# Kernel optimization log

Hardware: AMD Instinct MI355X
Metric: run time of the kernel (lower is better)

Reference implementation:

```python
import jax, jax.numpy as jnp
import numpy as np

N_TOTAL = 204800  # total valid nodes across the batch
B = 1024          # number of graphs
D = 512           # input_dim (dim_node)
H = 512           # hidden width of NonLinearClassifier
C = 52            # num_classes
EPS = 1e-5        # BatchNorm eps


def setup_inputs() -> dict:
    key = jax.random.key(0)
    kz, k1, k2, k3 = jax.random.split(key, 4)
    # ragged per-graph node counts summing exactly to N_TOTAL
    rng = np.random.default_rng(0)
    counts = rng.integers(50, 350, size=B).astype(np.float64)
    counts = np.floor(counts * N_TOTAL / counts.sum()).astype(np.int64)
    counts[-1] += N_TOTAL - counts.sum()
    assert counts.min() > 0 and counts.sum() == N_TOTAL
    return {
        "z": jax.random.normal(kz, (N_TOTAL, D), dtype=jnp.float32),
        "batch_num_nodes": jnp.asarray(counts, dtype=jnp.int64),
        "w1": jax.random.normal(k1, (D, H), dtype=jnp.float32) * 0.02,
        "b1": jnp.zeros((H,), jnp.float32),
        "g1": jnp.ones((H,), jnp.float32),
        "beta1": jnp.zeros((H,), jnp.float32),
        "w2": jax.random.normal(k2, (H, H), dtype=jnp.float32) * 0.02,
        "b2": jnp.zeros((H,), jnp.float32),
        "g2": jnp.ones((H,), jnp.float32),
        "beta2": jnp.zeros((H,), jnp.float32),
        "w3": jax.random.normal(k3, (H, C), dtype=jnp.float32) * 0.02,
        "b3": jnp.zeros((C,), jnp.float32),
    }


def _batchnorm(x, gamma, beta):
    # training-mode BatchNorm1d: batch statistics (biased variance)
    m = x.mean(axis=0)
    v = x.var(axis=0)
    return gamma * (x - m) * jax.lax.rsqrt(v + EPS) + beta


def reference(z, batch_num_nodes, w1, b1, g1, beta1, w2, b2, g2, beta2, w3, b3):
    # fused segment-mean pooling (replaces torch.split + per-graph .mean loop)
    seg_ids = jnp.repeat(jnp.arange(B), batch_num_nodes, total_repeat_length=N_TOTAL)
    sums = jax.ops.segment_sum(z, seg_ids, num_segments=B)          # [B, D]
    graph_feats = sums / batch_num_nodes.astype(z.dtype)[:, None]   # [B, D]
    # NonLinearClassifier MLP (dropout inactive in eval / deterministic ref)
    h = jax.nn.relu(_batchnorm(graph_feats @ w1 + b1, g1, beta1))
    h = jax.nn.relu(_batchnorm(h @ w2 + b2, g2, beta2))
    return h @ w3 + b3  # [B, C] logits
```

## Files before the change

kernel.cpp:

```cpp
#include <hip/hip_runtime.h>

#define N_TOTAL 204800
#define NB 1024
#define DIM 512
#define NC 52
#define BN_EPS 1e-5f

__device__ inline void f4add(float4& a, const float4 b) {
    a.x += b.x; a.y += b.y; a.z += b.z; a.w += b.w;
}

__device__ inline float bn_relu1(float v, int f,
                                 const float* __restrict__ s1, const float* __restrict__ s2,
                                 const float* __restrict__ g, const float* __restrict__ beta) {
    float m  = s1[f] * (1.0f / NB);
    float vv = s2[f] * (1.0f / NB) - m * m;
    float is = rsqrtf(vv + BN_EPS);
    float h  = g[f] * (v - m) * is + beta[f];
    return h > 0.f ? h : 0.f;
}

__global__ __launch_bounds__(1024) void k_scan(const int* __restrict__ bnn,
                                               int* __restrict__ offs,
                                               int* __restrict__ cnt,
                                               float* __restrict__ inv,
                                               float* __restrict__ stats ) {
    __shared__ int red[1024];
    int tid = threadIdx.x;
    int v32 = bnn[tid];
    red[tid] = v32;
    __syncthreads();
    for (int s = 512; s > 0; s >>= 1) {
        if (tid < s) red[tid] += red[tid + s];
        __syncthreads();
    }
    int total = red[0];
    __syncthreads();
    int c = (total == N_TOTAL) ? v32 : bnn[2 * tid];
    red[tid] = c;
    __syncthreads();
    for (int off = 1; off < 1024; off <<= 1) {
        int t = (tid >= off) ? red[tid - off] : 0;
        __syncthreads();
        red[tid] += t;
        __syncthreads();
    }
    offs[tid] = red[tid] - c;
    cnt[tid]  = c;
    inv[tid]  = 1.0f / (float)c;
    stats[tid]        = 0.0f;
    stats[tid + 1024] = 0.0f;
}

__global__ __launch_bounds__(256) void k_pool(const float* __restrict__ z,
                                              const int* __restrict__ offs,
                                              const int* __restrict__ cnt,
                                              const float* __restrict__ inv,
                                              float* __restrict__ X) {
    __shared__ float4 buf[3][32];
    int g  = blockIdx.x;
    int cc = blockIdx.y;
    int s0 = offs[g];
    int n  = cnt[g];
    float r = inv[g];
    int tid = threadIdx.x;
    int c4 = tid & 31;
    int rp = tid >> 5;
    const float4* p = (const float4*)z + (size_t)s0 * 128 + cc * 32 + c4;
    float4 a0 = {0,0,0,0}, a1 = {0,0,0,0}, a2 = {0,0,0,0}, a3 = {0,0,0,0};
    int i = rp;
    for (; i + 56 < n; i += 64) {
        float4 v0 = p[(size_t)(i +  0) * 128];
        float4 v1 = p[(size_t)(i +  8) * 128];
        float4 v2 = p[(size_t)(i + 16) * 128];
        float4 v3 = p[(size_t)(i + 24) * 128];
        float4 v4 = p[(size_t)(i + 32) * 128];
        float4 v5 = p[(size_t)(i + 40) * 128];
        float4 v6 = p[(size_t)(i + 48) * 128];
        float4 v7 = p[(size_t)(i + 56) * 128];
        f4add(a0, v0); f4add(a1, v1); f4add(a2, v2); f4add(a3, v3);
        f4add(a0, v4); f4add(a1, v5); f4add(a2, v6); f4add(a3, v7);
    }
    for (; i < n; i += 8) { float4 v = p[(size_t)i * 128]; f4add(a0, v); }
    f4add(a0, a1); f4add(a2, a3); f4add(a0, a2);
    a0.x += __shfl_xor(a0.x, 32); a0.y += __shfl_xor(a0.y, 32);
    a0.z += __shfl_xor(a0.z, 32); a0.w += __shfl_xor(a0.w, 32);
    int w    = tid >> 6;
    int lane = tid & 63;
    if (w > 0 && lane < 32) buf[w - 1][c4] = a0;
    __syncthreads();
    if (w == 0 && lane < 32) {
        f4add(a0, buf[0][c4]); f4add(a0, buf[1][c4]); f4add(a0, buf[2][c4]);
        a0.x *= r; a0.y *= r; a0.z *= r; a0.w *= r;
        ((float4*)X)[(size_t)g * 128 + cc * 32 + c4] = a0;
    }
}

template <bool BNA>
__global__ __launch_bounds__(256) void k_gemm32x64(const float* __restrict__ A,
                                                   const float* __restrict__ W,
                                                   const float* __restrict__ bias,
                                                   const float* __restrict__ ps1,
                                                   const float* __restrict__ ps2,
                                                   const float* __restrict__ gam,
                                                   const float* __restrict__ bet,
                                                   float* __restrict__ Y,
                                                   float* __restrict__ os1,
                                                   float* __restrict__ os2) {
    __shared__ float As[32][34];
    __shared__ float Ws[32][68];
    int tid = threadIdx.x;
    int tx = tid & 15, ty = tid >> 4;
    int gr0 = blockIdx.x * 32;
    int gc0 = blockIdx.y * 64;

    int arow = tid >> 3;
    int akq  = tid & 7;
    int wk0 = tid >> 4;
    int wcq = tid & 15;

    float acc[2][4] = {};

    float4 ra  = *(const float4*)&A[(size_t)(gr0 + arow) * DIM + akq * 4];
    float4 rw0 = *(const float4*)&W[(size_t)wk0 * DIM + gc0 + wcq * 4];
    float4 rw1 = *(const float4*)&W[(size_t)(wk0 + 16) * DIM + gc0 + wcq * 4];

    for (int kt = 0; kt < 16; kt++) {
        float4 v = ra;
        if (BNA) {
            int f0 = kt * 32 + akq * 4;
            v.x = bn_relu1(v.x, f0 + 0, ps1, ps2, gam, bet);
            v.y = bn_relu1(v.y, f0 + 1, ps1, ps2, gam, bet);
            v.z = bn_relu1(v.z, f0 + 2, ps1, ps2, gam, bet);
            v.w = bn_relu1(v.w, f0 + 3, ps1, ps2, gam, bet);
        }
        As[akq * 4 + 0][arow] = v.x;
        As[akq * 4 + 1][arow] = v.y;
        As[akq * 4 + 2][arow] = v.z;
        As[akq * 4 + 3][arow] = v.w;
        *(float4*)&Ws[wk0][wcq * 4]      = rw0;
        *(float4*)&Ws[wk0 + 16][wcq * 4] = rw1;
        __syncthreads();

        if (kt < 15) {
            int k0 = (kt + 1) * 32;
            ra  = *(const float4*)&A[(size_t)(gr0 + arow) * DIM + k0 + akq * 4];
            rw0 = *(const float4*)&W[(size_t)(k0 + wk0) * DIM + gc0 + wcq * 4];
            rw1 = *(const float4*)&W[(size_t)(k0 + wk0 + 16) * DIM + gc0 + wcq * 4];
        }

#pragma unroll
        for (int k = 0; k < 32; k++) {
            float2 a = *(const float2*)&As[k][ty * 2];
            float4 w = *(const float4*)&Ws[k][tx * 4];
            acc[0][0] += a.x * w.x; acc[0][1] += a.x * w.y;
            acc[0][2] += a.x * w.z; acc[0][3] += a.x * w.w;
            acc[1][0] += a.y * w.x; acc[1][1] += a.y * w.y;
            acc[1][2] += a.y * w.z; acc[1][3] += a.y * w.w;
        }
        __syncthreads();
    }

    float4 b = *(const float4*)&bias[gc0 + tx * 4];
    float s[4] = {}, q[4] = {};
#pragma unroll
    for (int i = 0; i < 2; i++) {
        float4 y;
        y.x = acc[i][0] + b.x;
        y.y = acc[i][1] + b.y;
        y.z = acc[i][2] + b.z;
        y.w = acc[i][3] + b.w;
        *(float4*)&Y[(size_t)(gr0 + ty * 2 + i) * DIM + gc0 + tx * 4] = y;
        s[0] += y.x; q[0] += y.x * y.x;
        s[1] += y.y; q[1] += y.y * y.y;
        s[2] += y.z; q[2] += y.z * y.z;
        s[3] += y.w; q[3] += y.w * y.w;
    }
#pragma unroll
    for (int j = 0; j < 4; j++) {
        s[j] += __shfl_xor(s[j], 16); s[j] += __shfl_xor(s[j], 32);
        q[j] += __shfl_xor(q[j], 16); q[j] += __shfl_xor(q[j], 32);
    }
    if ((ty & 3) == 0) {
#pragma unroll
        for (int j = 0; j < 4; j++) {
            atomicAdd(&os1[gc0 + tx * 4 + j], s[j]);
            atomicAdd(&os2[gc0 + tx * 4 + j], q[j]);
        }
    }
}

__global__ __launch_bounds__(256) void k_gemm3(const float* __restrict__ Y2,
                                               const float* __restrict__ W,
                                               const float* __restrict__ bias,
                                               const float* __restrict__ s1,
                                               const float* __restrict__ s2,
                                               const float* __restrict__ gam,
                                               const float* __restrict__ bet,
                                               float* __restrict__ out) {
    __shared__ float As[4][DIM];
    int tid = threadIdx.x;
    int r0 = blockIdx.x * 4;
#pragma unroll
    for (int it = 0; it < 2; it++) {
        int idx = it * 256 + tid;
        int row = idx >> 7;
        int cq  = idx & 127;
        int f   = cq * 4;
        float4 v = *(const float4*)&Y2[(size_t)(r0 + row) * DIM + f];
        v.x = bn_relu1(v.x, f + 0, s1, s2, gam, bet);
        v.y = bn_relu1(v.y, f + 1, s1, s2, gam, bet);
        v.z = bn_relu1(v.z, f + 2, s1, s2, gam, bet);
        v.w = bn_relu1(v.w, f + 3, s1, s2, gam, bet);
        *(float4*)&As[row][f] = v;
    }
    __syncthreads();
    int col = tid & 63;
    int row = tid >> 6;
    if (col < NC) {
        float acc = 0.f;
#pragma unroll 8
        for (int k = 0; k < DIM; k += 4) {
            float4 a = *(const float4*)&As[row][k];
            acc += a.x * W[(size_t)(k + 0) * NC + col];
            acc += a.y * W[(size_t)(k + 1) * NC + col];
            acc += a.z * W[(size_t)(k + 2) * NC + col];
            acc += a.w * W[(size_t)(k + 3) * NC + col];
        }
        out[(size_t)(r0 + row) * NC + col] = acc + bias[col];
    }
}

extern "C" void kernel_launch(void* const* d_in, const int* in_sizes, int n_in,
                              void* d_out, int out_size, void* d_ws, size_t ws_size,
                              hipStream_t stream) {
    const float* z   = (const float*)d_in[0];
    const int*   bnn = (const int*)d_in[1];
    const float* w1  = (const float*)d_in[2];
    const float* b1  = (const float*)d_in[3];
    const float* g1  = (const float*)d_in[4];
    const float* be1 = (const float*)d_in[5];
    const float* w2  = (const float*)d_in[6];
    const float* b2  = (const float*)d_in[7];
    const float* g2  = (const float*)d_in[8];
    const float* be2 = (const float*)d_in[9];
    const float* w3  = (const float*)d_in[10];
    const float* b3  = (const float*)d_in[11];

    int*   offs  = (int*)d_ws;
    int*   cnt   = offs + 1024;
    float* inv   = (float*)(cnt + 1024);
    float* stats = inv + 1024;
    float* X     = stats + 2048;
    float* Y1    = X  + (size_t)NB * DIM;
    float* Y2    = Y1 + (size_t)NB * DIM;
    float* out   = (float*)d_out;

    k_scan<<<1, 1024, 0, stream>>>(bnn, offs, cnt, inv, stats);
    k_pool<<<dim3(NB, 4), 256, 0, stream>>>(z, offs, cnt, inv, X);

    dim3 gg(NB / 32, DIM / 64);
    k_gemm32x64<false><<<gg, 256, 0, stream>>>(X, w1, b1,
                                               nullptr, nullptr, nullptr, nullptr,
                                               Y1, stats, stats + 512);
    k_gemm32x64<true><<<gg, 256, 0, stream>>>(Y1, w2, b2,
                                              stats, stats + 512, g1, be1,
                                              Y2, stats + 1024, stats + 1536);
    k_gemm3<<<NB / 4, 256, 0, stream>>>(Y2, w3, b3,
                                        stats + 1024, stats + 1536, g2, be2, out);
}
```

Measured before the change: 645.8 us.

## Use nontemporal loads in pooling, wave-shuffle scan, and 512-thread GEMM blocks

The pooling kernel now reads z with nontemporal vector loads, so the single-use 400MB stream bypasses cache retention. The scan kernel replaces its shared-memory tree reduction and prefix scan with wave-level shuffles plus a small cross-wave pass, which removes many barriers. The two hidden-layer GEMMs move to 512 threads per block, with each thread computing a 2x2 output tile instead of 2x4. That roughly halves per-thread work and raises occupancy, at the cost of half the threads sitting idle during A-tile loads and more atomics for the batch-norm statistics.

Measured after the change: 623.5 us. 1.04x faster.

```diff
diff --git a/kernel.cpp b/kernel.cpp
--- a/kernel.cpp
+++ b/kernel.cpp
@@ -5,6 +5,8 @@
 #define DIM 512
 #define NC 52
 #define BN_EPS 1e-5f
+
+typedef float nf4 __attribute__((ext_vector_type(4)));
 
 __device__ inline void f4add(float4& a, const float4 b) {
     a.x += b.x; a.y += b.y; a.z += b.z; a.w += b.w;
@@ -25,27 +27,34 @@
                                                int* __restrict__ cnt,
                                                float* __restrict__ inv,
                                                float* __restrict__ stats ) {
-    __shared__ int red[1024];
-    int tid = threadIdx.x;
-    int v32 = bnn[tid];
-    red[tid] = v32;
-    __syncthreads();
-    for (int s = 512; s > 0; s >>= 1) {
-        if (tid < s) red[tid] += red[tid + s];
-        __syncthreads();
-    }
-    int total = red[0];
-    __syncthreads();
+    __shared__ int wtot[16];
+    __shared__ int wsum[16];
+    int tid  = threadIdx.x;
+    int lane = tid & 63;
+    int w    = tid >> 6;
+    int v32  = bnn[tid];
+    int t = v32;
+#pragma unroll
+    for (int s = 1; s < 64; s <<= 1) t += __shfl_xor(t, s);
+    if (lane == 0) wtot[w] = t;
+    __syncthreads();
+    int total = 0;
+#pragma unroll
+    for (int i = 0; i < 16; i++) total += wtot[i];
     int c = (total == N_TOTAL) ? v32 : bnn[2 * tid];
-    red[tid] = c;
-    __syncthreads();
-    for (int off = 1; off < 1024; off <<= 1) {
-        int t = (tid >= off) ? red[tid - off] : 0;
-        __syncthreads();
-        red[tid] += t;
-        __syncthreads();
-    }
-    offs[tid] = red[tid] - c;
+    int x = c;
+#pragma unroll
+    for (int s = 1; s < 64; s <<= 1) {
+        int u = __shfl_up(x, s);
+        if (lane >= s) x += u;
+    }
+    if (lane == 63) wsum[w] = x;
+    __syncthreads();
+    int pre = 0;
+#pragma unroll
+    for (int i = 0; i < 16; i++) if (i < w) pre += wsum[i];
+    int incl = pre + x;
+    offs[tid] = incl - c;
     cnt[tid]  = c;
     inv[tid]  = 1.0f / (float)c;
     stats[tid]        = 0.0f;
@@ -57,7 +66,7 @@
                                               const int* __restrict__ cnt,
                                               const float* __restrict__ inv,
                                               float* __restrict__ X) {
-    __shared__ float4 buf[3][32];
+    __shared__ nf4 buf[3][32];
     int g  = blockIdx.x;
     int cc = blockIdx.y;
     int s0 = offs[g];
@@ -66,23 +75,25 @@
     int tid = threadIdx.x;
     int c4 = tid & 31;
     int rp = tid >> 5;
-    const float4* p = (const float4*)z + (size_t)s0 * 128 + cc * 32 + c4;
-    float4 a0 = {0,0,0,0}, a1 = {0,0,0,0}, a2 = {0,0,0,0}, a3 = {0,0,0,0};
+    const nf4* p = (const nf4*)z + (size_t)s0 * 128 + cc * 32 + c4;
+    nf4 a0 = {0,0,0,0}, a1 = {0,0,0,0}, a2 = {0,0,0,0}, a3 = {0,0,0,0};
     int i = rp;
     for (; i + 56 < n; i += 64) {
-        float4 v0 = p[(size_t)(i +  0) * 128];
-        float4 v1 = p[(size_t)(i +  8) * 128];
-        float4 v2 = p[(size_t)(i + 16) * 128];
-        float4 v3 = p[(size_t)(i + 24) * 128];
-        float4 v4 = p[(size_t)(i + 32) * 128];
-        float4 v5 = p[(size_t)(i + 40) * 128];
-        float4 v6 = p[(size_t)(i + 48) * 128];
-        float4 v7 = p[(size_t)(i + 56) * 128];
-        f4add(a0, v0); f4add(a1, v1); f4add(a2, v2); f4add(a3, v3);
-        f4add(a0, v4); f4add(a1, v5); f4add(a2, v6); f4add(a3, v7);
-    }
-    for (; i < n; i += 8) { float4 v = p[(size_t)i * 128]; f4add(a0, v); }
-    f4add(a0, a1); f4add(a2, a3); f4add(a0, a2);
+        nf4 v0 = __builtin_nontemporal_load(&p[(size_t)(i +  0) * 128]);
+        nf4 v1 = __builtin_nontemporal_load(&p[(size_t)(i +  8) * 128]);
+        nf4 v2 = __builtin_nontemporal_load(&p[(size_t)(i + 16) * 128]);
+        nf4 v3 = __builtin_nontemporal_load(&p[(size_t)(i + 24) * 128]);
+        nf4 v4 = __builtin_nontemporal_load(&p[(size_t)(i + 32) * 128]);
+        nf4 v5 = __builtin_nontemporal_load(&p[(size_t)(i + 40) * 128]);
+        nf4 v6 = __builtin_nontemporal_load(&p[(size_t)(i + 48) * 128]);
+        nf4 v7 = __builtin_nontemporal_load(&p[(size_t)(i + 56) * 128]);
+        a0 += v0; a1 += v1; a2 += v2; a3 += v3;
+        a0 += v4; a1 += v5; a2 += v6; a3 += v7;
+    }
+    for (; i < n; i += 8) {
+        a0 += __builtin_nontemporal_load(&p[(size_t)i * 128]);
+    }
+    a0 += a1; a2 += a3; a0 += a2;
     a0.x += __shfl_xor(a0.x, 32); a0.y += __shfl_xor(a0.y, 32);
     a0.z += __shfl_xor(a0.z, 32); a0.w += __shfl_xor(a0.w, 32);
     int w    = tid >> 6;
@@ -90,14 +101,14 @@
     if (w > 0 && lane < 32) buf[w - 1][c4] = a0;
     __syncthreads();
     if (w == 0 && lane < 32) {
-        f4add(a0, buf[0][c4]); f4add(a0, buf[1][c4]); f4add(a0, buf[2][c4]);
-        a0.x *= r; a0.y *= r; a0.z *= r; a0.w *= r;
-        ((float4*)X)[(size_t)g * 128 + cc * 32 + c4] = a0;
+        a0 += buf[0][c4]; a0 += buf[1][c4]; a0 += buf[2][c4];
+        a0 *= r;
+        ((nf4*)X)[(size_t)g * 128 + cc * 32 + c4] = a0;
     }
 }
 
 template <bool BNA>
-__global__ __launch_bounds__(256) void k_gemm32x64(const float* __restrict__ A,
+__global__ __launch_bounds__(512) void k_gemm32x64(const float* __restrict__ A,
                                                    const float* __restrict__ W,
                                                    const float* __restrict__ bias,
                                                    const float* __restrict__ ps1,
@@ -110,83 +121,74 @@
     __shared__ float As[32][34];
     __shared__ float Ws[32][68];
     int tid = threadIdx.x;
-    int tx = tid & 15, ty = tid >> 4;
+    int tx = tid & 31, ty = tid >> 5;
     int gr0 = blockIdx.x * 32;
     int gc0 = blockIdx.y * 64;
 
-    int arow = tid >> 3;
+    int arow = (tid & 255) >> 3;
     int akq  = tid & 7;
-    int wk0 = tid >> 4;
+    int wk  = tid >> 4;
     int wcq = tid & 15;
 
-    float acc[2][4] = {};
-
-    float4 ra  = *(const float4*)&A[(size_t)(gr0 + arow) * DIM + akq * 4];
-    float4 rw0 = *(const float4*)&W[(size_t)wk0 * DIM + gc0 + wcq * 4];
-    float4 rw1 = *(const float4*)&W[(size_t)(wk0 + 16) * DIM + gc0 + wcq * 4];
+    float acc[2][2] = {};
+
+    float4 ra = {0, 0, 0, 0};
+    if (tid < 256) ra = *(const float4*)&A[(size_t)(gr0 + arow) * DIM + akq * 4];
+    float4 rw = *(const float4*)&W[(size_t)wk * DIM + gc0 + wcq * 4];
 
     for (int kt = 0; kt < 16; kt++) {
-        float4 v = ra;
-        if (BNA) {
-            int f0 = kt * 32 + akq * 4;
-            v.x = bn_relu1(v.x, f0 + 0, ps1, ps2, gam, bet);
-            v.y = bn_relu1(v.y, f0 + 1, ps1, ps2, gam, bet);
-            v.z = bn_relu1(v.z, f0 + 2, ps1, ps2, gam, bet);
-            v.w = bn_relu1(v.w, f0 + 3, ps1, ps2, gam, bet);
-        }
-        As[akq * 4 + 0][arow] = v.x;
-        As[akq * 4 + 1][arow] = v.y;
-        As[akq * 4 + 2][arow] = v.z;
-        As[akq * 4 + 3][arow] = v.w;
-        *(float4*)&Ws[wk0][wcq * 4]      = rw0;
-        *(float4*)&Ws[wk0 + 16][wcq * 4] = rw1;
+        if (tid < 256) {
+            float4 v = ra;
+            if (BNA) {
+                int f0 = kt * 32 + akq * 4;
+                v.x = bn_relu1(v.x, f0 + 0, ps1, ps2, gam, bet);
+                v.y = bn_relu1(v.y, f0 + 1, ps1, ps2, gam, bet);
+                v.z = bn_relu1(v.z, f0 + 2, ps1, ps2, gam, bet);
+                v.w = bn_relu1(v.w, f0 + 3, ps1, ps2, gam, bet);
+            }
+            As[akq * 4 + 0][arow] = v.x;
+            As[akq * 4 + 1][arow] = v.y;
+            As[akq * 4 + 2][arow] = v.z;
+            As[akq * 4 + 3][arow] = v.w;
+        }
+        *(float4*)&Ws[wk][wcq * 4] = rw;
         __syncthreads();
 
         if (kt < 15) {
             int k0 = (kt + 1) * 32;
-            ra  = *(const float4*)&A[(size_t)(gr0 + arow) * DIM + k0 + akq * 4];
-            rw0 = *(const float4*)&W[(size_t)(k0 + wk0) * DIM + gc0 + wcq * 4];
-            rw1 = *(const float4*)&W[(size_t)(k0 + wk0 + 16) * DIM + gc0 + wcq * 4];
+            if (tid < 256)
+                ra = *(const float4*)&A[(size_t)(gr0 + arow) * DIM + k0 + akq * 4];
+            rw = *(const float4*)&W[(size_t)(k0 + wk) * DIM + gc0 + wcq * 4];
         }
 
 #pragma unroll
         for (int k = 0; k < 32; k++) {
             float2 a = *(const float2*)&As[k][ty * 2];
-            float4 w = *(const float4*)&Ws[k][tx * 4];
+            float2 w = *(const float2*)&Ws[k][tx * 2];
             acc[0][0] += a.x * w.x; acc[0][1] += a.x * w.y;
-            acc[0][2] += a.x * w.z; acc[0][3] += a.x * w.w;
             acc[1][0] += a.y * w.x; acc[1][1] += a.y * w.y;
-            acc[1][2] += a.y * w.z; acc[1][3] += a.y * w.w;
         }
         __syncthreads();
     }
 
-    float4 b = *(const float4*)&bias[gc0 + tx * 4];
-    float s[4] = {}, q[4] = {};
+    float2 b = *(const float2*)&bias[gc0 + tx * 2];
+    float s0 = 0, s1 = 0, q0 = 0, q1 = 0;
 #pragma unroll
     for (int i = 0; i < 2; i++) {
-        float4 y;
+        float2 y;
         y.x = acc[i][0] + b.x;
         y.y = acc[i][1] + b.y;
-        y.z = acc[i][2] + b.z;
-        y.w = acc[i][3] + b.w;
-        *(float4*)&Y[(size_t)(gr0 + ty * 2 + i) * DIM + gc0 + tx * 4] = y;
-        s[0] += y.x; q[0] += y.x * y.x;
-        s[1] += y.y; q[1] += y.y * y.y;
-        s[2] += y.z; q[2] += y.z * y.z;
-        s[3] += y.w; q[3] += y.w * y.w;
-    }
-#pragma unroll
-    for (int j = 0; j < 4; j++) {
-        s[j] += __shfl_xor(s[j], 16); s[j] += __shfl_xor(s[j], 32);
-        q[j] += __shfl_xor(q[j], 16); q[j] += __shfl_xor(q[j], 32);
-    }
-    if ((ty & 3) == 0) {
-#pragma unroll
-        for (int j = 0; j < 4; j++) {
-            atomicAdd(&os1[gc0 + tx * 4 + j], s[j]);
-            atomicAdd(&os2[gc0 + tx * 4 + j], q[j]);
-        }
+        *(float2*)&Y[(size_t)(gr0 + ty * 2 + i) * DIM + gc0 + tx * 2] = y;
+        s0 += y.x; q0 += y.x * y.x;
+        s1 += y.y; q1 += y.y * y.y;
+    }
+    s0 += __shfl_xor(s0, 32); q0 += __shfl_xor(q0, 32);
+    s1 += __shfl_xor(s1, 32); q1 += __shfl_xor(q1, 32);
+    if ((tid & 63) < 32) {
+        atomicAdd(&os1[gc0 + tx * 2 + 0], s0);
+        atomicAdd(&os1[gc0 + tx * 2 + 1], s1);
+        atomicAdd(&os2[gc0 + tx * 2 + 0], q0);
+        atomicAdd(&os2[gc0 + tx * 2 + 1], q1);
     }
 }
 
@@ -260,10 +262,10 @@
     k_pool<<<dim3(NB, 4), 256, 0, stream>>>(z, offs, cnt, inv, X);
 
     dim3 gg(NB / 32, DIM / 64);
-    k_gemm32x64<false><<<gg, 256, 0, stream>>>(X, w1, b1,
+    k_gemm32x64<false><<<gg, 512, 0, stream>>>(X, w1, b1,
                                                nullptr, nullptr, nullptr, nullptr,
                                                Y1, stats, stats + 512);
-    k_gemm32x64<true><<<gg, 256, 0, stream>>>(Y1, w2, b2,
+    k_gemm32x64<true><<<gg, 512, 0, stream>>>(Y1, w2, b2,
                                               stats, stats + 512, g1, be1,
                                               Y2, stats + 1024, stats + 1536);
     k_gemm3<<<NB / 4, 256, 0, stream>>>(Y2, w3, b3,
```
